# Kernel tuning notes

Hardware: AMD Instinct MI355X
Metric: run time of the kernel (lower is better)

## Reference

```python
import jax, jax.numpy as jnp
import numpy as np

NUM_HEADS = 8
BLOCK = 16
EPS = 1e-5


def setup_inputs() -> dict:
    key = jax.random.key(0)
    ks = jax.random.split(key, 5)
    B, C, H, W = 2, 256, 192, 192
    x = jax.random.normal(ks[0], (B, C, H, W), dtype=jnp.float32)
    s = 1.0 / np.sqrt(C).astype(np.float32)
    Wq = jax.random.normal(ks[1], (C, C), dtype=jnp.float32) * s
    Wk = jax.random.normal(ks[2], (C, C), dtype=jnp.float32) * s
    Wv = jax.random.normal(ks[3], (C, C), dtype=jnp.float32) * s
    Wo = jax.random.normal(ks[4], (C, C), dtype=jnp.float32) * s
    gamma = jnp.ones((C,), dtype=jnp.float32)
    beta = jnp.zeros((C,), dtype=jnp.float32)
    return {"x": x, "Wq": Wq, "Wk": Wk, "Wv": Wv, "Wo": Wo, "gamma": gamma, "beta": beta}


def _to_blocks(t, B, nH, d, H, W, bs):
    # [B, C, H, W] -> [B, nH, n_blocks, bs*bs, d]
    nbh, nbw = H // bs, W // bs
    t = t.reshape(B, nH, d, nbh, bs, nbw, bs)
    t = t.transpose(0, 1, 3, 5, 4, 6, 2)  # B nH nbh nbw bs bs d
    return t.reshape(B, nH, nbh * nbw, bs * bs, d)


def _from_blocks(t, B, nH, d, H, W, bs):
    # [B, nH, n_blocks, bs*bs, d] -> [B, C, H, W]
    nbh, nbw = H // bs, W // bs
    t = t.reshape(B, nH, nbh, nbw, bs, bs, d)
    t = t.transpose(0, 1, 6, 2, 4, 3, 5)  # B nH d nbh bs nbw bs
    return t.reshape(B, nH * d, H, W)


def reference(x, Wq, Wk, Wv, Wo, gamma, beta):
    B, C, H, W = x.shape
    nH, bs = NUM_HEADS, BLOCK
    d = C // nH
    scale = 1.0 / np.float32(np.sqrt(d))

    # 1x1 convs == channel matmuls
    q = jnp.einsum('bchw,oc->bohw', x, Wq)
    k = jnp.einsum('bchw,oc->bohw', x, Wk)
    v = jnp.einsum('bchw,oc->bohw', x, Wv)

    qb = _to_blocks(q, B, nH, d, H, W, bs)
    kb = _to_blocks(k, B, nH, d, H, W, bs)
    vb = _to_blocks(v, B, nH, d, H, W, bs)

    # block-local attention: i,j index the bs*bs pixels inside a block
    scores = jnp.einsum('bnkid,bnkjd->bnkij', qb, kb) * scale
    attn = jax.nn.softmax(scores, axis=-1)
    o = jnp.einsum('bnkij,bnkjd->bnkid', attn, vb)

    o = _from_blocks(o, B, nH, d, H, W, bs)
    o = jnp.einsum('bchw,oc->bohw', o, Wo) + x  # output projection + residual

    # LayerNorm over channels
    mu = jnp.mean(o, axis=1, keepdims=True)
    var = jnp.var(o, axis=1, keepdims=True)
    o = (o - mu) * jax.lax.rsqrt(var + EPS)
    return o * gamma[None, :, None, None] + beta[None, :, None, None]
```

## Files before the change

kernel.cpp:

```cpp
#include <hip/hip_runtime.h>
#include <hip/hip_bf16.h>

namespace {

constexpr int kC    = 256;
constexpr int kH    = 192, kW = 192;
constexpr int kHW   = kH * kW;
constexpr int kNBD  = 12;
constexpr int kNBLK = kNBD * kNBD;

typedef __attribute__((ext_vector_type(8))) short          bf16x8;
typedef __attribute__((ext_vector_type(8))) unsigned short u16x8;
typedef __attribute__((ext_vector_type(4))) unsigned short u16x4;
typedef __attribute__((ext_vector_type(4))) float          f32x4;

__device__ __forceinline__ unsigned short f2bf(float f) {
  union { float f; unsigned u; } x; x.f = f;
  unsigned r = x.u + 0x7fffu + ((x.u >> 16) & 1u);
  return (unsigned short)(r >> 16);
}

__device__ __forceinline__ unsigned pack_bf16(float lo, float hi) {
  return (unsigned)f2bf(lo) | ((unsigned)f2bf(hi) << 16);
}

__device__ __forceinline__ f32x4 mfma16(bf16x8 a, bf16x8 b, f32x4 c) {
  return __builtin_amdgcn_mfma_f32_16x16x32_bf16(a, b, c, 0, 0, 0);
}

__global__ void k_convw(const float* __restrict__ wq, const float* __restrict__ wk,
                        const float* __restrict__ wv, const float* __restrict__ wo,
                        unsigned short* __restrict__ dst) {
  int i = blockIdx.x * 256 + threadIdx.x;
  const float* s = (blockIdx.y == 0) ? wq : (blockIdx.y == 1) ? wk
                 : (blockIdx.y == 2) ? wv : wo;
  dst[(size_t)blockIdx.y * 65536 + i] = f2bf(s[i]);
}

__global__ __launch_bounds__(256, 3)
void k_qkv(const float* __restrict__ x, const unsigned short* __restrict__ wbf,
           unsigned short* __restrict__ qw, unsigned short* __restrict__ kw,
           unsigned short* __restrict__ vw) {
  __shared__ unsigned short xTs[64 * 256];
  __shared__ unsigned short oT[32 * 256];
  const int tid = threadIdx.x;
  const int w = tid >> 6, l = tid & 63;
  const int m0 = blockIdx.x * 64;
  const int b  = m0 / kHW;
  const int px0 = m0 % kHW;

  {
    const float* xb = x + (size_t)b * kC * kHW + px0;
    #pragma unroll
    for (int i = 0; i < 64; i += 2) {
      const int c = w * 64 + i;
      float f0 = xb[(size_t)c * kHW + l];
      float f1 = xb[(size_t)(c + 1) * kHW + l];
      unsigned pk = pack_bf16(f0, f1);
      const int cb = c >> 3;
      const int col = ((cb ^ (l & 7)) << 3) + (c & 7);
      *(unsigned*)&xTs[l * 256 + col] = pk;
    }
  }
  __syncthreads();

  const int l15 = l & 15, l4 = l >> 4;

  for (int mat = 0; mat < 3; ++mat) {
    const unsigned short* wmat = wbf + (size_t)mat * 65536;
    f32x4 acc[4][4];
    #pragma unroll
    for (int ot = 0; ot < 4; ++ot)
      #pragma unroll
      for (int pt = 0; pt < 4; ++pt)
        acc[ot][pt] = (f32x4){0.f, 0.f, 0.f, 0.f};

    #pragma unroll
    for (int kc = 0; kc < 8; ++kc) {
      bf16x8 af[4], bf[4];
      #pragma unroll
      for (int ot = 0; ot < 4; ++ot)
        af[ot] = *(const bf16x8*)&wmat[(size_t)(w * 64 + ot * 16 + l15) * 256 + kc * 32 + l4 * 8];
      #pragma unroll
      for (int pt = 0; pt < 4; ++pt) {
        const int cb = kc * 4 + l4;
        bf[pt] = *(const bf16x8*)&xTs[(pt * 16 + l15) * 256 + ((cb ^ (l15 & 7)) << 3)];
      }
      #pragma unroll
      for (int ot = 0; ot < 4; ++ot)
        #pragma unroll
        for (int pt = 0; pt < 4; ++pt)
          acc[ot][pt] = mfma16(af[ot], bf[pt], acc[ot][pt]);
    }

    unsigned short* dst = (mat == 0 ? qw : (mat == 1 ? kw : vw)) + ((size_t)b * kHW + px0) * 256;
    for (int h = 0; h < 2; ++h) {
      __syncthreads();
      #pragma unroll
      for (int pp = 0; pp < 2; ++pp) {
        const int pt  = 2 * h + pp;
        const int row = pp * 16 + l15;
        #pragma unroll
        for (int ot = 0; ot < 4; ++ot) {
          const f32x4 a = acc[ot][pt];
          u16x4 pk;
          #pragma unroll
          for (int r = 0; r < 4; ++r) pk[r] = f2bf(a[r]);
          const int bb = w * 8 + ot * 2 + (l4 >> 1);
          *(u16x4*)&oT[row * 256 + ((bb ^ (row & 7)) << 3) + (l4 & 1) * 4] = pk;
        }
      }
      __syncthreads();
      const int row2 = tid >> 3, ocb = tid & 7;
      #pragma unroll
      for (int k2 = 0; k2 < 4; ++k2) {
        const int bb2 = ocb * 4 + k2;
        u16x8 vv = *(const u16x8*)&oT[row2 * 256 + ((bb2 ^ (row2 & 7)) << 3)];
        *(u16x8*)&dst[(size_t)(h * 32 + row2) * 256 + ocb * 32 + k2 * 8] = vv;
      }
    }
  }
}

__global__ __launch_bounds__(512, 2)
void k_attn(const unsigned short* __restrict__ qw, const unsigned short* __restrict__ kw,
            const unsigned short* __restrict__ vw, unsigned short* __restrict__ ow) {
  __shared__ unsigned short P[256][264];
  __shared__ unsigned short T[32][264];
  const int tid = threadIdx.x;
  int bx = blockIdx.x;
  const int blk = bx % kNBLK; bx /= kNBLK;
  const int head = bx & 7; const int b = bx >> 3;
  const int bh = blk / kNBD, bw = blk % kNBD;
  const int px00 = bh * 16 * kW + bw * 16;
  const size_t base = ((size_t)b * kHW) * 256 + head * 32;

  {
    const int j = tid >> 1, half = tid & 1;
    const int px = px00 + (j >> 4) * kW + (j & 15);
    const unsigned short* vp = vw + base + (size_t)px * 256 + half * 16;
    u16x8 a = *(const u16x8*)&vp[0];
    u16x8 c = *(const u16x8*)&vp[8];
    #pragma unroll
    for (int e = 0; e < 8; ++e) {
      T[half * 16 + e][j]     = a[e];
      T[half * 16 + 8 + e][j] = c[e];
    }
  }

  const int lane = tid & 63, wave = tid >> 6;
  const int l15 = lane & 15, l4 = lane >> 4;
  const f32x4 fz = {0.f, 0.f, 0.f, 0.f};

  bf16x8 qfr[2];
  #pragma unroll
  for (int it = 0; it < 2; ++it) {
    const int i  = wave * 32 + it * 16 + l15;
    const int px = px00 + (i >> 4) * kW + (i & 15);
    qfr[it] = *(const bf16x8*)&qw[base + (size_t)px * 256 + l4 * 8];
  }
  f32x4 s[16][2];
  #pragma unroll
  for (int jt = 0; jt < 16; ++jt) {
    const int px = px00 + jt * kW + l15;
    bf16x8 kf = *(const bf16x8*)&kw[base + (size_t)px * 256 + l4 * 8];
    s[jt][0] = mfma16(kf, qfr[0], fz);
    s[jt][1] = mfma16(kf, qfr[1], fz);
  }

  const float sc = 0.17677669529663687f;
  #pragma unroll
  for (int it = 0; it < 2; ++it) {
    float m = -3.0e38f;
    #pragma unroll
    for (int jt = 0; jt < 16; ++jt)
      #pragma unroll
      for (int r = 0; r < 4; ++r)
        m = fmaxf(m, s[jt][it][r]);
    m = fmaxf(m, __shfl_xor(m, 16));
    m = fmaxf(m, __shfl_xor(m, 32));
    float su = 0.f;
    #pragma unroll
    for (int jt = 0; jt < 16; ++jt)
      #pragma unroll
      for (int r = 0; r < 4; ++r) {
        float e = __expf((s[jt][it][r] - m) * sc);
        s[jt][it][r] = e;
        su += e;
      }
    su += __shfl_xor(su, 16);
    su += __shfl_xor(su, 32);
    const float inv = 1.f / su;
    const int i = wave * 32 + it * 16 + l15;
    #pragma unroll
    for (int jt = 0; jt < 16; ++jt) {
      u16x4 pk;
      #pragma unroll
      for (int r = 0; r < 4; ++r) pk[r] = f2bf(s[jt][it][r] * inv);
      *(u16x4*)&P[i][jt * 16 + l4 * 4] = pk;
    }
  }
  __syncthreads();

  f32x4 oa[2][2];
  oa[0][0] = fz; oa[0][1] = fz; oa[1][0] = fz; oa[1][1] = fz;
  #pragma unroll
  for (int kt = 0; kt < 8; ++kt) {
    bf16x8 av0 = *(const bf16x8*)&T[l15][kt * 32 + l4 * 8];
    bf16x8 av1 = *(const bf16x8*)&T[16 + l15][kt * 32 + l4 * 8];
    bf16x8 bp0 = *(const bf16x8*)&P[wave * 32 + l15][kt * 32 + l4 * 8];
    bf16x8 bp1 = *(const bf16x8*)&P[wave * 32 + 16 + l15][kt * 32 + l4 * 8];
    oa[0][0] = mfma16(av0, bp0, oa[0][0]);
    oa[0][1] = mfma16(av0, bp1, oa[0][1]);
    oa[1][0] = mfma16(av1, bp0, oa[1][0]);
    oa[1][1] = mfma16(av1, bp1, oa[1][1]);
  }
  __syncthreads();
  #pragma unroll
  for (int ddt = 0; ddt < 2; ++ddt)
    #pragma unroll
    for (int it = 0; it < 2; ++it)
      #pragma unroll
      for (int r = 0; r < 4; ++r)
        T[ddt * 16 + l4 * 4 + r][wave * 32 + it * 16 + l15] = f2bf(oa[ddt][it][r]);
  __syncthreads();
  {
    const int i = tid >> 1, half = tid & 1;
    const int px = px00 + (i >> 4) * kW + (i & 15);
    u16x8 w0, w1;
    #pragma unroll
    for (int e = 0; e < 8; ++e) {
      w0[e] = T[half * 16 + e][i];
      w1[e] = T[half * 16 + 8 + e][i];
    }
    unsigned short* op = ow + base + (size_t)px * 256 + half * 16;
    *(u16x8*)&op[0] = w0;
    *(u16x8*)&op[8] = w1;
  }
}

__global__ __launch_bounds__(256, 3)
void k_proj_ln(const unsigned short* __restrict__ oatt, const unsigned short* __restrict__ wo,
               const float* __restrict__ x, const float* __restrict__ gamma,
               const float* __restrict__ beta, float* __restrict__ out) {
  __shared__ float pa[4][64], pb[4][64];
  const int tid = threadIdx.x, w = tid >> 6, lane = tid & 63;
  const int l15 = lane & 15, l4 = lane >> 4;
  const int m0 = blockIdx.x * 64;
  const int b = m0 / kHW, px0 = m0 % kHW;

  f32x4 acc[4][4];
  #pragma unroll
  for (int ot = 0; ot < 4; ++ot)
    #pragma unroll
    for (int pt = 0; pt < 4; ++pt)
      acc[ot][pt] = (f32x4){0.f, 0.f, 0.f, 0.f};

  const unsigned short* ob = oatt + ((size_t)b * kHW + px0) * 256;
  for (int kc = 0; kc < 8; ++kc) {
    bf16x8 bfr[4];
    #pragma unroll
    for (int pt = 0; pt < 4; ++pt)
      bfr[pt] = *(const bf16x8*)&ob[(size_t)(pt * 16 + l15) * 256 + kc * 32 + l4 * 8];
    #pragma unroll
    for (int ot = 0; ot < 4; ++ot) {
      bf16x8 af = *(const bf16x8*)&wo[(size_t)(w * 64 + ot * 16 + l15) * 256 + kc * 32 + l4 * 8];
      #pragma unroll
      for (int pt = 0; pt < 4; ++pt)
        acc[ot][pt] = mfma16(af, bfr[pt], acc[ot][pt]);
    }
  }

  const float* xb = x + (size_t)b * kC * kHW + px0;
  float s1[4] = {0.f, 0.f, 0.f, 0.f}, s2[4] = {0.f, 0.f, 0.f, 0.f};
  #pragma unroll
  for (int ot = 0; ot < 4; ++ot)
    #pragma unroll
    for (int r = 0; r < 4; ++r) {
      const int oc = w * 64 + ot * 16 + l4 * 4 + r;
      #pragma unroll
      for (int pt = 0; pt < 4; ++pt) {
        float v = acc[ot][pt][r] + xb[(size_t)oc * kHW + pt * 16 + l15];
        acc[ot][pt][r] = v;
        s1[pt] += v;
        s2[pt] += v * v;
      }
    }
  #pragma unroll
  for (int pt = 0; pt < 4; ++pt) {
    s1[pt] += __shfl_xor(s1[pt], 16);
    s1[pt] += __shfl_xor(s1[pt], 32);
    s2[pt] += __shfl_xor(s2[pt], 16);
    s2[pt] += __shfl_xor(s2[pt], 32);
  }
  if (l4 == 0) {
    #pragma unroll
    for (int pt = 0; pt < 4; ++pt) {
      pa[w][pt * 16 + l15] = s1[pt];
      pb[w][pt * 16 + l15] = s2[pt];
    }
  }
  __syncthreads();
  float mean[4], rstd[4];
  #pragma unroll
  for (int pt = 0; pt < 4; ++pt) {
    const int px = pt * 16 + l15;
    float a = pa[0][px] + pa[1][px] + pa[2][px] + pa[3][px];
    float q = pb[0][px] + pb[1][px] + pb[2][px] + pb[3][px];
    mean[pt] = a * (1.f / 256.f);
    float var = q * (1.f / 256.f) - mean[pt] * mean[pt];
    rstd[pt] = rsqrtf(var + 1e-5f);
  }
  float* outb = out + (size_t)b * kC * kHW + px0;
  #pragma unroll
  for (int ot = 0; ot < 4; ++ot)
    #pragma unroll
    for (int r = 0; r < 4; ++r) {
      const int oc = w * 64 + ot * 16 + l4 * 4 + r;
      const float g = gamma[oc], be = beta[oc];
      #pragma unroll
      for (int pt = 0; pt < 4; ++pt)
        outb[(size_t)oc * kHW + pt * 16 + l15] = (acc[ot][pt][r] - mean[pt]) * rstd[pt] * g + be;
    }
}

}

extern "C" void kernel_launch(void* const* d_in, const int* in_sizes, int n_in,
                              void* d_out, int out_size, void* d_ws, size_t ws_size,
                              hipStream_t stream) {
  const float* x     = (const float*)d_in[0];
  const float* Wq    = (const float*)d_in[1];
  const float* Wk    = (const float*)d_in[2];
  const float* Wv    = (const float*)d_in[3];
  const float* Wo    = (const float*)d_in[4];
  const float* gamma = (const float*)d_in[5];
  const float* beta  = (const float*)d_in[6];
  float* out = (float*)d_out;

  const int nbatch = 2;
  const size_t per = (size_t)nbatch * kHW * 256;

  unsigned short* wbf = (unsigned short*)d_ws;
  unsigned short* qws = wbf + 4 * 65536;
  unsigned short* kws = qws + per;
  unsigned short* vws = kws + per;
  unsigned short* ows = qws;

  k_convw<<<dim3(256, 4), 256, 0, stream>>>(Wq, Wk, Wv, Wo, wbf);
  k_qkv<<<(nbatch * kHW) / 64, 256, 0, stream>>>(x, wbf, qws, kws, vws);
  k_attn<<<nbatch * 8 * kNBLK, 512, 0, stream>>>(qws, kws, vws, ows);
  k_proj_ln<<<(nbatch * kHW) / 64, 256, 0, stream>>>(ows, wbf + 3 * 65536, x, gamma, beta, out);
}
```

Before: 247.8 us.

## Stage LN output through swizzled LDS for vectorized stores; batch x loads

```diff
diff --git a/kernel.cpp b/kernel.cpp
--- a/kernel.cpp
+++ b/kernel.cpp
@@ -52,14 +52,19 @@
   {
     const float* xb = x + (size_t)b * kC * kHW + px0;
     #pragma unroll
-    for (int i = 0; i < 64; i += 2) {
-      const int c = w * 64 + i;
-      float f0 = xb[(size_t)c * kHW + l];
-      float f1 = xb[(size_t)(c + 1) * kHW + l];
-      unsigned pk = pack_bf16(f0, f1);
-      const int cb = c >> 3;
-      const int col = ((cb ^ (l & 7)) << 3) + (c & 7);
-      *(unsigned*)&xTs[l * 256 + col] = pk;
+    for (int chunk = 0; chunk < 4; ++chunk) {
+      float v[16];
+      #pragma unroll
+      for (int i = 0; i < 16; ++i)
+        v[i] = xb[(size_t)(w * 64 + chunk * 16 + i) * kHW + l];
+      #pragma unroll
+      for (int i = 0; i < 16; i += 2) {
+        const int c = w * 64 + chunk * 16 + i;
+        unsigned pk = pack_bf16(v[i], v[i + 1]);
+        const int cb = c >> 3;
+        const int col = ((cb ^ (l & 7)) << 3) + (c & 7);
+        *(unsigned*)&xTs[l * 256 + col] = pk;
+      }
     }
   }
   __syncthreads();
@@ -239,10 +244,11 @@
   }
 }
 
-__global__ __launch_bounds__(256, 3)
+__global__ __launch_bounds__(256, 4)
 void k_proj_ln(const unsigned short* __restrict__ oatt, const unsigned short* __restrict__ wo,
                const float* __restrict__ x, const float* __restrict__ gamma,
                const float* __restrict__ beta, float* __restrict__ out) {
+  __shared__ float oT[128 * 64];
   __shared__ float pa[4][64], pb[4][64];
   const int tid = threadIdx.x, w = tid >> 6, lane = tid & 63;
   const int l15 = lane & 15, l4 = lane >> 4;
@@ -311,17 +317,39 @@
     float var = q * (1.f / 256.f) - mean[pt] * mean[pt];
     rstd[pt] = rsqrtf(var + 1e-5f);
   }
+
   float* outb = out + (size_t)b * kC * kHW + px0;
-  #pragma unroll
-  for (int ot = 0; ot < 4; ++ot)
-    #pragma unroll
-    for (int r = 0; r < 4; ++r) {
-      const int oc = w * 64 + ot * 16 + l4 * 4 + r;
-      const float g = gamma[oc], be = beta[oc];
-      #pragma unroll
-      for (int pt = 0; pt < 4; ++pt)
-        outb[(size_t)oc * kHW + pt * 16 + l15] = (acc[ot][pt][r] - mean[pt]) * rstd[pt] * g + be;
-    }
+  for (int h = 0; h < 2; ++h) {
+    __syncthreads();
+    #pragma unroll
+    for (int ot2 = 0; ot2 < 2; ++ot2) {
+      const int ot = 2 * h + ot2;
+      #pragma unroll
+      for (int r = 0; r < 4; ++r) {
+        const int lrow = w * 32 + ot2 * 16 + l4 * 4 + r;
+        const int oc   = w * 64 + ot * 16 + l4 * 4 + r;
+        const int swz  = ((lrow & 3) ^ ((lrow >> 2) & 3)) << 2;
+        const float g = gamma[oc], be = beta[oc];
+        #pragma unroll
+        for (int pt = 0; pt < 4; ++pt) {
+          const int p   = pt * 16 + l15;
+          const int col = (((p >> 2) ^ swz) << 2) + (p & 3);
+          oT[lrow * 64 + col] = (acc[ot][pt][r] - mean[pt]) * rstd[pt] * g + be;
+        }
+      }
+    }
+    __syncthreads();
+    const int seg = tid & 15;
+    #pragma unroll
+    for (int it2 = 0; it2 < 8; ++it2) {
+      const int lrow = (tid >> 4) + it2 * 16;
+      const int swz  = ((lrow & 3) ^ ((lrow >> 2) & 3)) << 2;
+      f32x4 vv = *(const f32x4*)&oT[lrow * 64 + ((seg ^ swz) << 2)];
+      const int w2  = lrow >> 5, rem = lrow & 31;
+      const int oc  = w2 * 64 + (2 * h + (rem >> 4)) * 16 + (rem & 15);
+      *(f32x4*)&outb[(size_t)oc * kHW + seg * 4] = vv;
+    }
+  }
 }
 
 }
```

After: 275.3 us. +11.1%, slower.
